# Optimization experiments

Hardware: AMD Instinct MI355X
Metric: run time of the kernel (lower is better)

## Reference

```python
import jax, jax.numpy as jnp
import numpy as np

HIDDEN = 64
CLASSES = 5


def setup_inputs() -> dict:
    key = jax.random.key(0)
    ks = jax.random.split(key, 7)
    B, T = 512, 3600
    s = 1.0 / np.sqrt(HIDDEN)  # PyTorch GRU init scale
    x = jax.random.normal(ks[0], (B, T, 1), dtype=jnp.float32)
    w_ih = jax.random.uniform(ks[1], (3 * HIDDEN, 1), jnp.float32, -s, s)
    w_hh = jax.random.uniform(ks[2], (3 * HIDDEN, HIDDEN), jnp.float32, -s, s)
    b_ih = jax.random.uniform(ks[3], (3 * HIDDEN,), jnp.float32, -s, s)
    b_hh = jax.random.uniform(ks[4], (3 * HIDDEN,), jnp.float32, -s, s)
    w_head = jax.random.uniform(ks[5], (CLASSES, HIDDEN), jnp.float32, -s, s)
    b_head = jax.random.uniform(ks[6], (CLASSES,), jnp.float32, -s, s)
    return {"x": x, "w_ih": w_ih, "w_hh": w_hh, "b_ih": b_ih,
            "b_hh": b_hh, "w_head": w_head, "b_head": b_head}


def reference(x, w_ih, w_hh, b_ih, b_hh, w_head, b_head):
    # x: [B, T, 1]; single-layer GRU (PyTorch gate ordering r, z, n), h0 = 0.
    B, T, _ = x.shape
    H = w_hh.shape[1]
    # Precompute input projections for all timesteps: [T, B, 3H]
    gi = jnp.einsum('bti,gi->tbg', x, w_ih) + b_ih

    def step(h, gi_t):
        gh = h @ w_hh.T + b_hh                      # [B, 3H]
        i_r, i_z, i_n = jnp.split(gi_t, 3, axis=-1)
        h_r, h_z, h_n = jnp.split(gh, 3, axis=-1)
        r = jax.nn.sigmoid(i_r + h_r)
        z = jax.nn.sigmoid(i_z + h_z)
        n = jnp.tanh(i_n + r * h_n)
        h_new = (1.0 - z) * n + z * h
        return h_new, None

    h0 = jnp.zeros((B, H), dtype=x.dtype)
    h_last, _ = jax.lax.scan(step, h0, gi)
    # head on last hidden state: [B, classes]
    return h_last @ w_head.T + b_head
```

## Files before the change

### kernel.cpp

```cpp
#include <hip/hip_runtime.h>

#define BATCH   512
#define GB      4
#define NBLK    (BATCH / GB)
#define TSTEPS  3600
#define H       64
#define XCHUNK  16
#define NCHUNK  (TSTEPS / XCHUNK)
#define CLASSES 5

typedef _Float16 half8 __attribute__((ext_vector_type(8)));
typedef float    f32x4 __attribute__((ext_vector_type(4)));

#define L2E 1.44269504088896f
#define S_N (2.0f * L2E)

__device__ __forceinline__ half8 bc_h8(uint4 v) { return __builtin_bit_cast(half8, v); }

__global__ __launch_bounds__(256, 1) void gru_mfma_kernel(
    const float* __restrict__ x,
    const float* __restrict__ w_ih,
    const float* __restrict__ w_hh,
    const float* __restrict__ b_ih,
    const float* __restrict__ b_hh,
    const float* __restrict__ w_head,
    const float* __restrict__ b_head,
    float* __restrict__ out)
{
    __shared__ __align__(16) _Float16 hB[2][GB * 80];
    __shared__ float hf[GB][H];

    const int tid  = threadIdx.x;
    const int w    = tid >> 6;
    const int lane = tid & 63;
    const int q    = lane >> 4;
    const int col  = lane & 15;
    const int b0   = blockIdx.x * GB;
    const int i    = 16 * w + col;

    half8 wR[2], wZ[2], wN[2];
#pragma unroll
    for (int c = 0; c < 2; ++c) {
        const float* pr = w_hh + (16 * w       + col) * H + 32 * c + 8 * q;
        const float* pz = w_hh + (16 * (4 + w) + col) * H + 32 * c + 8 * q;
        const float* pn = w_hh + (16 * (8 + w) + col) * H + 32 * c + 8 * q;
        half8 fr, fz, fn;
#pragma unroll
        for (int j = 0; j < 8; ++j) {
            fr[j] = (_Float16)(-L2E * pr[j]);
            fz[j] = (_Float16)(-L2E * pz[j]);
            fn[j] = (_Float16)( S_N * pn[j]);
        }
        wR[c] = fr; wZ[c] = fz; wN[c] = fn;
    }

    const float bn = S_N * b_hh[2 * H + i];
    f32x4 Cn = {bn, bn, bn, bn};
    const f32x4 Z = {0.f, 0.f, 0.f, 0.f};
    f32x4 Cr = Z, Cz = Z;

    const float wih_r = -L2E * w_ih[i];
    const float wih_z = -L2E * w_ih[H + i];
    const float wih_n =  S_N * w_ih[2 * H + i];
    const float bsr = -L2E * (b_ih[i] + b_hh[i]);
    const float bsz = -L2E * (b_ih[H + i] + b_hh[H + i]);
    const float bin =  S_N * b_ih[2 * H + i];

    char* hbase = (char*)&hB[0][0];
    const int rdA0 = (col >> 2) * 160 + q * 16;
    const int rdA1 = rdA0 + 64;
    const int wrH  = q * 160 + i * 2;

    *(_Float16*)(hbase + wrH) = (_Float16)0.0f;
    __syncthreads();

    const float* xq = x + (size_t)(b0 + q) * TSTEPS;
    float vx = xq[col];
    const int pbase = 64 * q;

    float xt0 = __builtin_bit_cast(float,
        __builtin_amdgcn_ds_bpermute(pbase, __builtin_bit_cast(int, vx)));
    float irc = fmaf(xt0, wih_r, bsr);
    float izc = fmaf(xt0, wih_z, bsz);
    float inc = fmaf(xt0, wih_n, bin);

    float h_reg = 0.0f, hm1 = -1.0f;

    for (int tc = 0; tc < NCHUNK; ++tc) {
        const int nb = (tc + 1 < NCHUNK) ? (tc + 1) * XCHUNK : 0;
        const float vxn = xq[nb + col];

#pragma unroll
        for (int tt = 0; tt < XCHUNK; ++tt) {
            const int pr_ = (tt & 1) * 640;
            const int pw_ = ((tt & 1) ^ 1) * 640;

            const uint4 a0 = *(const uint4*)(hbase + pr_ + rdA0);
            const uint4 a1 = *(const uint4*)(hbase + pr_ + rdA1);

            const float xsrc = (tt == XCHUNK - 1) ? vxn : vx;
            const float xtn = __builtin_bit_cast(float,
                __builtin_amdgcn_ds_bpermute(pbase + 4 * ((tt + 1) & 15),
                                             __builtin_bit_cast(int, xsrc)));

            Cr[0] = irc;
            Cz[0] = izc;

            const half8 A0 = bc_h8(a0);
            const half8 A1 = bc_h8(a1);
            f32x4 dr, dn, dz;
            dr = __builtin_amdgcn_mfma_f32_16x16x32_f16(A0, wR[0], Cr, 0, 0, 0);
            dr = __builtin_amdgcn_mfma_f32_16x16x32_f16(A1, wR[1], dr, 0, 0, 0);
            dn = __builtin_amdgcn_mfma_f32_16x16x32_f16(A0, wN[0], Cn, 0, 0, 0);
            dn = __builtin_amdgcn_mfma_f32_16x16x32_f16(A1, wN[1], dn, 0, 0, 0);
            dz = __builtin_amdgcn_mfma_f32_16x16x32_f16(A0, wZ[0], Cz, 0, 0, 0);
            dz = __builtin_amdgcn_mfma_f32_16x16x32_f16(A1, wZ[1], dz, 0, 0, 0);

            const float er = __builtin_amdgcn_exp2f(dr[0]);
            const float r  = __builtin_amdgcn_rcpf(1.0f + er);
            const float ev = __builtin_amdgcn_exp2f(fmaf(r, dn[0], inc));
            const float u  = __builtin_amdgcn_rcpf(ev + 1.0f);
            const float nn = fmaf(-2.0f, u, 1.0f);
            const float s  = fmaf(2.0f, u, hm1);
            const float ez = __builtin_amdgcn_exp2f(dz[0]);
            const float zg = __builtin_amdgcn_rcpf(1.0f + ez);
            h_reg = fmaf(zg, s, nn);
            hm1   = h_reg - 1.0f;

            irc = fmaf(xtn, wih_r, bsr);
            izc = fmaf(xtn, wih_z, bsz);
            inc = fmaf(xtn, wih_n, bin);

            *(_Float16*)(hbase + pw_ + wrH) = (_Float16)h_reg;
            __syncthreads();
        }
        vx = vxn;
    }

    hf[q][i] = h_reg;
    __syncthreads();
    {
        const float hv = hf[w][lane];
#pragma unroll
        for (int cc = 0; cc < CLASSES; ++cc) {
            float v = hv * w_head[cc * H + lane];
#pragma unroll
            for (int off = 32; off > 0; off >>= 1)
                v += __shfl_down(v, off, 64);
            if (lane == 0) out[(b0 + w) * CLASSES + cc] = v + b_head[cc];
        }
    }
}

extern "C" void kernel_launch(void* const* d_in, const int* in_sizes, int n_in,
                              void* d_out, int out_size, void* d_ws, size_t ws_size,
                              hipStream_t stream) {
    const float* x      = (const float*)d_in[0];
    const float* w_ih   = (const float*)d_in[1];
    const float* w_hh   = (const float*)d_in[2];
    const float* b_ih   = (const float*)d_in[3];
    const float* b_hh   = (const float*)d_in[4];
    const float* w_head = (const float*)d_in[5];
    const float* b_head = (const float*)d_in[6];
    float* out = (float*)d_out;

    gru_mfma_kernel<<<NBLK, 256, 0, stream>>>(x, w_ih, w_hh, b_ih, b_hh,
                                              w_head, b_head, out);
}
```

Before: 721.1 us.

## Split MFMA accumulation chains and load x as vector registers per chunk

Each gate's two chained MFMAs become two independent MFMAs whose results are summed in scalar code. This shortens the dependent MFMA latency on the serial recurrence path. The x inputs are now loaded with 16-wide vector loads into double-buffered registers instead of being broadcast with ds_bpermute each step, which removes one LDS permute per step. The cost is three extra MFMAs' worth of accumulator registers and an extra add per gate, plus more VGPRs for the x buffers.

```diff
diff --git a/kernel.cpp b/kernel.cpp
--- a/kernel.cpp
+++ b/kernel.cpp
@@ -55,9 +55,9 @@
     }
 
     const float bn = S_N * b_hh[2 * H + i];
-    f32x4 Cn = {bn, bn, bn, bn};
-    const f32x4 Z = {0.f, 0.f, 0.f, 0.f};
-    f32x4 Cr = Z, Cz = Z;
+    const f32x4 Cn = {bn, bn, bn, bn};
+    const f32x4 Z  = {0.f, 0.f, 0.f, 0.f};
+    f32x4 CrV = Z, CzV = Z;
 
     const float wih_r = -L2E * w_ih[i];
     const float wih_z = -L2E * w_ih[H + i];
@@ -75,67 +75,61 @@
     __syncthreads();
 
     const float* xq = x + (size_t)(b0 + q) * TSTEPS;
-    float vx = xq[col];
-    const int pbase = 64 * q;
-
-    float xt0 = __builtin_bit_cast(float,
-        __builtin_amdgcn_ds_bpermute(pbase, __builtin_bit_cast(int, vx)));
-    float irc = fmaf(xt0, wih_r, bsr);
-    float izc = fmaf(xt0, wih_z, bsz);
-    float inc = fmaf(xt0, wih_n, bin);
+    f32x4 xe0, xe1, xe2, xe3, xo0, xo1, xo2, xo3;
+    xe0 = *(const f32x4*)(xq);      xe1 = *(const f32x4*)(xq + 4);
+    xe2 = *(const f32x4*)(xq + 8);  xe3 = *(const f32x4*)(xq + 12);
 
     float h_reg = 0.0f, hm1 = -1.0f;
 
+#define STEP(tt, XT) {                                                         \
+    const int pr_ = ((tt) & 1) * 640;                                          \
+    const int pw_ = (((tt) & 1) ^ 1) * 640;                                    \
+    const uint4 a0 = *(const uint4*)(hbase + pr_ + rdA0);                      \
+    const uint4 a1 = *(const uint4*)(hbase + pr_ + rdA1);                      \
+    const float xt_ = (XT);                                                    \
+    CrV[0] = fmaf(xt_, wih_r, bsr);                  \
+    CzV[0] = fmaf(xt_, wih_z, bsz);                                            \
+    const float inc = fmaf(xt_, wih_n, bin);                                   \
+    const half8 A0 = bc_h8(a0), A1 = bc_h8(a1);                                \
+    f32x4 r0 = __builtin_amdgcn_mfma_f32_16x16x32_f16(A0, wR[0], CrV, 0,0,0);  \
+    f32x4 r1 = __builtin_amdgcn_mfma_f32_16x16x32_f16(A1, wR[1], Z,   0,0,0);  \
+    f32x4 n0 = __builtin_amdgcn_mfma_f32_16x16x32_f16(A0, wN[0], Cn,  0,0,0);  \
+    f32x4 n1 = __builtin_amdgcn_mfma_f32_16x16x32_f16(A1, wN[1], Z,   0,0,0);  \
+    f32x4 z0 = __builtin_amdgcn_mfma_f32_16x16x32_f16(A0, wZ[0], CzV, 0,0,0);  \
+    f32x4 z1 = __builtin_amdgcn_mfma_f32_16x16x32_f16(A1, wZ[1], Z,   0,0,0);  \
+    const float er = __builtin_amdgcn_exp2f(r0[0] + r1[0]);                    \
+    const float rr = __builtin_amdgcn_rcpf(1.0f + er);                         \
+    const float ev = __builtin_amdgcn_exp2f(fmaf(rr, n0[0] + n1[0], inc));     \
+    const float uu = __builtin_amdgcn_rcpf(ev + 1.0f);                         \
+    const float nn = fmaf(-2.0f, uu, 1.0f);                          \
+    const float ss = fmaf(2.0f, uu, hm1);                          \
+    const float ez = __builtin_amdgcn_exp2f(z0[0] + z1[0]);                    \
+    const float zg = __builtin_amdgcn_rcpf(1.0f + ez);                         \
+    h_reg = fmaf(zg, ss, nn);                                 \
+    hm1 = h_reg - 1.0f;                                                        \
+    *(_Float16*)(hbase + pw_ + wrH) = (_Float16)h_reg;                         \
+    __syncthreads(); }
+
+#define STEPS16(V0, V1, V2, V3)                                                \
+    STEP(0,  V0[0]) STEP(1,  V0[1]) STEP(2,  V0[2]) STEP(3,  V0[3])            \
+    STEP(4,  V1[0]) STEP(5,  V1[1]) STEP(6,  V1[2]) STEP(7,  V1[3])            \
+    STEP(8,  V2[0]) STEP(9,  V2[1]) STEP(10, V2[2]) STEP(11, V2[3])            \
+    STEP(12, V3[0]) STEP(13, V3[1]) STEP(14, V3[2]) STEP(15, V3[3])
+
     for (int tc = 0; tc < NCHUNK; ++tc) {
-        const int nb = (tc + 1 < NCHUNK) ? (tc + 1) * XCHUNK : 0;
-        const float vxn = xq[nb + col];
-
-#pragma unroll
-        for (int tt = 0; tt < XCHUNK; ++tt) {
-            const int pr_ = (tt & 1) * 640;
-            const int pw_ = ((tt & 1) ^ 1) * 640;
-
-            const uint4 a0 = *(const uint4*)(hbase + pr_ + rdA0);
-            const uint4 a1 = *(const uint4*)(hbase + pr_ + rdA1);
-
-            const float xsrc = (tt == XCHUNK - 1) ? vxn : vx;
-            const float xtn = __builtin_bit_cast(float,
-                __builtin_amdgcn_ds_bpermute(pbase + 4 * ((tt + 1) & 15),
-                                             __builtin_bit_cast(int, xsrc)));
-
-            Cr[0] = irc;
-            Cz[0] = izc;
-
-            const half8 A0 = bc_h8(a0);
-            const half8 A1 = bc_h8(a1);
-            f32x4 dr, dn, dz;
-            dr = __builtin_amdgcn_mfma_f32_16x16x32_f16(A0, wR[0], Cr, 0, 0, 0);
-            dr = __builtin_amdgcn_mfma_f32_16x16x32_f16(A1, wR[1], dr, 0, 0, 0);
-            dn = __builtin_amdgcn_mfma_f32_16x16x32_f16(A0, wN[0], Cn, 0, 0, 0);
-            dn = __builtin_amdgcn_mfma_f32_16x16x32_f16(A1, wN[1], dn, 0, 0, 0);
-            dz = __builtin_amdgcn_mfma_f32_16x16x32_f16(A0, wZ[0], Cz, 0, 0, 0);
-            dz = __builtin_amdgcn_mfma_f32_16x16x32_f16(A1, wZ[1], dz, 0, 0, 0);
-
-            const float er = __builtin_amdgcn_exp2f(dr[0]);
-            const float r  = __builtin_amdgcn_rcpf(1.0f + er);
-            const float ev = __builtin_amdgcn_exp2f(fmaf(r, dn[0], inc));
-            const float u  = __builtin_amdgcn_rcpf(ev + 1.0f);
-            const float nn = fmaf(-2.0f, u, 1.0f);
-            const float s  = fmaf(2.0f, u, hm1);
-            const float ez = __builtin_amdgcn_exp2f(dz[0]);
-            const float zg = __builtin_amdgcn_rcpf(1.0f + ez);
-            h_reg = fmaf(zg, s, nn);
-            hm1   = h_reg - 1.0f;
-
-            irc = fmaf(xtn, wih_r, bsr);
-            izc = fmaf(xtn, wih_z, bsz);
-            inc = fmaf(xtn, wih_n, bin);
-
-            *(_Float16*)(hbase + pw_ + wrH) = (_Float16)h_reg;
-            __syncthreads();
+        const float* nx = xq + ((tc + 1 < NCHUNK) ? (tc + 1) * XCHUNK : 0);
+        if ((tc & 1) == 0) {
+            xo0 = *(const f32x4*)(nx);      xo1 = *(const f32x4*)(nx + 4);
+            xo2 = *(const f32x4*)(nx + 8);  xo3 = *(const f32x4*)(nx + 12);
+            STEPS16(xe0, xe1, xe2, xe3)
+        } else {
+            xe0 = *(const f32x4*)(nx);      xe1 = *(const f32x4*)(nx + 4);
+            xe2 = *(const f32x4*)(nx + 8);  xe3 = *(const f32x4*)(nx + 12);
+            STEPS16(xo0, xo1, xo2, xo3)
         }
-        vx = vxn;
     }
+#undef STEPS16
+#undef STEP
 
     hf[q][i] = h_reg;
     __syncthreads();
```

Result: slower. 784.8 us (+8.8%).
